# Performance work log

Measured on AMD Instinct MI355X. Metric: run time of the kernel, lower is better.

## Reference

```python
import jax, jax.numpy as jnp
import numpy as np

N = 50000      # nodes
E = 800000     # edges (avg degree 32 w/ 50k nodes -> 16 per direction here)
IN = 128       # in_channels
H = 64         # hidden_channels
G = 64         # graphs in the batch
C = 2          # num_classes


def setup_inputs() -> dict:
    key = jax.random.key(0)
    ks = jax.random.split(key, 8)
    x = jax.random.normal(ks[0], (N, IN), dtype=jnp.float32)
    edge_index = jax.random.randint(ks[1], (2, E), 0, N, dtype=jnp.int64)
    batch = jnp.sort(jax.random.randint(ks[2], (N,), 0, G, dtype=jnp.int64))
    # learned parameters (glorot-ish scale)
    W1 = jax.random.normal(ks[3], (IN, H), dtype=jnp.float32) * (1.0 / np.sqrt(IN))
    b1 = jnp.zeros((H,), dtype=jnp.float32)
    W2 = jax.random.normal(ks[4], (H, H), dtype=jnp.float32) * (1.0 / np.sqrt(H))
    b2 = jnp.zeros((H,), dtype=jnp.float32)
    Wl = jax.random.normal(ks[5], (H, C), dtype=jnp.float32) * (1.0 / np.sqrt(H))
    bl = jnp.zeros((C,), dtype=jnp.float32)
    return {"x": x, "edge_index": edge_index, "batch": batch,
            "W1": W1, "b1": b1, "W2": W2, "b2": b2, "Wl": Wl, "bl": bl}


def _gcn_conv(x, src, dst, W, b, n):
    # PyG GCNConv: linear transform, add self-loops, sym-normalize, scatter-add at dst
    h = x @ W                                   # [n, H]
    loop = jnp.arange(n, dtype=src.dtype)
    s = jnp.concatenate([src, loop])            # [E+n]
    d = jnp.concatenate([dst, loop])
    deg = jax.ops.segment_sum(jnp.ones_like(d, dtype=h.dtype), d, num_segments=n)
    dinv = deg ** -0.5                          # deg >= 1 due to self-loops
    norm = dinv[s] * dinv[d]                    # [E+n]
    msg = h[s] * norm[:, None]                  # gather + scale
    out = jax.ops.segment_sum(msg, d, num_segments=n)  # scatter-add aggregate
    return out + b


def reference(x, edge_index, batch, W1, b1, W2, b2, Wl, bl):
    src, dst = edge_index[0], edge_index[1]
    h = jax.nn.relu(_gcn_conv(x, src, dst, W1, b1, N))
    # dropout is identity in eval mode
    h = jax.nn.relu(_gcn_conv(h, src, dst, W2, b2, N))
    # global mean pool per graph
    counts = jax.ops.segment_sum(jnp.ones((N,), dtype=h.dtype), batch, num_segments=G)
    pooled = jax.ops.segment_sum(h, batch, num_segments=G) / jnp.maximum(counts, 1.0)[:, None]
    out = pooled @ Wl + bl                      # [G, C]
    return (out, pooled)
```

## Files before the change

kernel.cpp:

```cpp
#include <hip/hip_runtime.h>

#define N_NODES   50000
#define N_EDGES   800000
#define IN_CH     128
#define HID       64
#define N_GRAPHS  64
#define N_CLASSES 2
#define NBLK_SCAN ((N_NODES + 255) / 256)
#define NREP      32


#define FILL_CHUNKS ((N_EDGES + 2047) / 2048)
__global__ __launch_bounds__(256) void deg_kernel(const int* __restrict__ ei,
                                                  int* __restrict__ degCount) {
    int part = blockIdx.x & 7;
    int blk  = blockIdx.x >> 3;
    int lo   = part * 6250;
    int hi   = lo + 6250;
#pragma unroll
    for (int it = 0; it < 8; ++it) {
        int e = blk * 2048 + it * 256 + (int)threadIdx.x;
        if (e < N_EDGES) {
            int dst = ei[N_EDGES + e];
            if (dst >= lo && dst < hi) atomicAdd(&degCount[dst], 1);
        }
    }
}

__global__ __launch_bounds__(256) void scan1_kernel(const int* __restrict__ degCount,
                                                    int* __restrict__ blockSums) {
    __shared__ int red[256];
    int i = blockIdx.x * 256 + threadIdx.x;
    red[threadIdx.x] = (i < N_NODES) ? degCount[i] : 0;
    __syncthreads();
    for (int off = 128; off > 0; off >>= 1) {
        if (threadIdx.x < off) red[threadIdx.x] += red[threadIdx.x + off];
        __syncthreads();
    }
    if (threadIdx.x == 0) blockSums[blockIdx.x] = red[0];
}

__global__ __launch_bounds__(256) void scan2_kernel(int* __restrict__ blockSums) {
    __shared__ int s[256];
    int t = threadIdx.x;
    int v = (t < NBLK_SCAN) ? blockSums[t] : 0;
    s[t] = v;
    __syncthreads();
    for (int off = 1; off < 256; off <<= 1) {
        int a = (t >= off) ? s[t - off] : 0;
        __syncthreads();
        s[t] += a;
        __syncthreads();
    }
    if (t < NBLK_SCAN) blockSums[t] = s[t] - v;
}

__global__ __launch_bounds__(256) void scan3_kernel(int* __restrict__ degFill,
                                                    const int* __restrict__ blockSums,
                                                    int* __restrict__ rowPtr,
                                                    float* __restrict__ dinv) {
    __shared__ int s[256];
    int t = threadIdx.x;
    int i = blockIdx.x * 256 + t;
    int d = (i < N_NODES) ? degFill[i] : 0;
    s[t] = d;
    __syncthreads();
    for (int off = 1; off < 256; off <<= 1) {
        int a = (t >= off) ? s[t - off] : 0;
        __syncthreads();
        s[t] += a;
        __syncthreads();
    }
    int excl = s[t] - d + blockSums[blockIdx.x];
    if (i < N_NODES) {
        rowPtr[i]  = excl;
        degFill[i] = excl;
        dinv[i]    = 1.0f / sqrtf((float)(d + 1));
    }
    if (i == 0) rowPtr[N_NODES] = N_EDGES;
}

__global__ __launch_bounds__(256) void fill_kernel(const int* __restrict__ ei,
                                                   int* __restrict__ fillPtr,
                                                   int* __restrict__ colIdx) {
    int part = blockIdx.x & 7;
    int blk  = blockIdx.x >> 3;
    int lo   = part * 6250;
    int hi   = lo + 6250;
#pragma unroll
    for (int it = 0; it < 8; ++it) {
        int e = blk * 2048 + it * 256 + (int)threadIdx.x;
        if (e < N_EDGES) {
            int dst = ei[N_EDGES + e];
            if (dst >= lo && dst < hi) {
                int src = ei[e];
                int pos = atomicAdd(&fillPtr[dst], 1);
                colIdx[pos] = src;
            }
        }
    }
}

#define FMA4(xs, w, a) { (a).x = fmaf((xs), (w).x, (a).x); \
                         (a).y = fmaf((xs), (w).y, (a).y); \
                         (a).z = fmaf((xs), (w).z, (a).z); \
                         (a).w = fmaf((xs), (w).w, (a).w); }

template <int K>
__global__ __launch_bounds__(256) void gemm_kernel(const float* __restrict__ A,
                                                   const float* __restrict__ W,
                                                   const float* __restrict__ dinv,
                                                   float* __restrict__ out) {
    __shared__ float4 Ws[K * 16];
    for (int i = threadIdx.x; i < K * 16; i += 256)
        Ws[i] = ((const float4*)W)[i];
    __syncthreads();

    const int c4   = threadIdx.x & 15;
    const int rg   = threadIdx.x >> 4;
    const int row0 = blockIdx.x * 128 + rg * 8;

    const float4* ap[8];
#pragma unroll
    for (int r = 0; r < 8; ++r) {
        int rowc = min(row0 + r, N_NODES - 1);
        ap[r] = (const float4*)(A + (size_t)rowc * K);
    }

    float4 acc[8] = {};
    for (int kk = 0; kk < K / 4; ++kk) {
        float4 xv[8];
#pragma unroll
        for (int r = 0; r < 8; ++r) xv[r] = ap[r][kk];
        float4 w;
        w = Ws[(4 * kk + 0) * 16 + c4];
#pragma unroll
        for (int r = 0; r < 8; ++r) FMA4(xv[r].x, w, acc[r]);
        w = Ws[(4 * kk + 1) * 16 + c4];
#pragma unroll
        for (int r = 0; r < 8; ++r) FMA4(xv[r].y, w, acc[r]);
        w = Ws[(4 * kk + 2) * 16 + c4];
#pragma unroll
        for (int r = 0; r < 8; ++r) FMA4(xv[r].z, w, acc[r]);
        w = Ws[(4 * kk + 3) * 16 + c4];
#pragma unroll
        for (int r = 0; r < 8; ++r) FMA4(xv[r].w, w, acc[r]);
    }

#pragma unroll
    for (int r = 0; r < 8; ++r) {
        int row = row0 + r;
        if (row < N_NODES) {
            float dv = dinv[row];
            float4 o = acc[r];
            o.x *= dv; o.y *= dv; o.z *= dv; o.w *= dv;
            ((float4*)(out + (size_t)row * HID))[c4] = o;
        }
    }
}

__global__ __launch_bounds__(256) void agg_kernel(const float* __restrict__ g,
                                                  const float* __restrict__ dinv,
                                                  const int* __restrict__ rowPtr,
                                                  const int* __restrict__ colIdx,
                                                  const float* __restrict__ bias,
                                                  float* __restrict__ out) {
    int lane = threadIdx.x & 63;
    int v = blockIdx.x * 4 + (threadIdx.x >> 6);
    if (v >= N_NODES) return;

    float acc = g[(size_t)v * HID + lane];
    int e  = rowPtr[v];
    int e1 = rowPtr[v + 1];
    for (; e + 3 < e1; e += 4) {
        int u0 = colIdx[e], u1 = colIdx[e + 1], u2 = colIdx[e + 2], u3 = colIdx[e + 3];
        float a0 = g[(size_t)u0 * HID + lane];
        float a1 = g[(size_t)u1 * HID + lane];
        float a2 = g[(size_t)u2 * HID + lane];
        float a3 = g[(size_t)u3 * HID + lane];
        acc += (a0 + a1) + (a2 + a3);
    }
    for (; e < e1; ++e) acc += g[(size_t)colIdx[e] * HID + lane];

    float r = dinv[v] * acc + bias[lane];
    out[(size_t)v * HID + lane] = fmaxf(r, 0.f);
}

__global__ __launch_bounds__(256) void agg2pool_kernel(const float* __restrict__ g,
                                                       const float* __restrict__ dinv,
                                                       const int* __restrict__ rowPtr,
                                                       const int* __restrict__ colIdx,
                                                       const float* __restrict__ bias,
                                                       const int* __restrict__ batch,
                                                       float* __restrict__ pooledSum) {
    int lane = threadIdx.x & 63;
    int v = blockIdx.x * 4 + (threadIdx.x >> 6);
    if (v >= N_NODES) return;

    float acc = g[(size_t)v * HID + lane];
    int e  = rowPtr[v];
    int e1 = rowPtr[v + 1];
    for (; e + 3 < e1; e += 4) {
        int u0 = colIdx[e], u1 = colIdx[e + 1], u2 = colIdx[e + 2], u3 = colIdx[e + 3];
        float a0 = g[(size_t)u0 * HID + lane];
        float a1 = g[(size_t)u1 * HID + lane];
        float a2 = g[(size_t)u2 * HID + lane];
        float a3 = g[(size_t)u3 * HID + lane];
        acc += (a0 + a1) + (a2 + a3);
    }
    for (; e < e1; ++e) acc += g[(size_t)colIdx[e] * HID + lane];

    float r = fmaxf(dinv[v] * acc + bias[lane], 0.f);
    int gid = batch[v];
    int rep = blockIdx.x & (NREP - 1);
    atomicAdd(&pooledSum[(size_t)rep * N_GRAPHS * HID + gid * HID + lane], r);
}

__global__ __launch_bounds__(64) void pool2_kernel(const float* __restrict__ pooledSum,
                                                   const int* __restrict__ batch,
                                                   const float* __restrict__ Wl,
                                                   const float* __restrict__ bl,
                                                   float* __restrict__ dout) {
    int g    = blockIdx.x;
    int lane = threadIdx.x;

    int lo0 = 0, hi = N_NODES;
    while (lo0 < hi) { int mid = (lo0 + hi) >> 1; if (batch[mid] < g) lo0 = mid + 1; else hi = mid; }
    int lo1 = lo0; hi = N_NODES;
    while (lo1 < hi) { int mid = (lo1 + hi) >> 1; if (batch[mid] < g + 1) lo1 = mid + 1; else hi = mid; }
    float cnt = (float)(lo1 - lo0);

    float s = 0.f;
#pragma unroll
    for (int rep = 0; rep < NREP; ++rep)
        s += pooledSum[(size_t)rep * N_GRAPHS * HID + g * HID + lane];

    float p = s / fmaxf(cnt, 1.0f);
    dout[N_GRAPHS * N_CLASSES + g * HID + lane] = p;

    float p0 = p * Wl[lane * N_CLASSES + 0];
    float p1 = p * Wl[lane * N_CLASSES + 1];
#pragma unroll
    for (int off = 32; off > 0; off >>= 1) {
        p0 += __shfl_down(p0, off, 64);
        p1 += __shfl_down(p1, off, 64);
    }
    if (lane == 0) {
        dout[g * N_CLASSES + 0] = p0 + bl[0];
        dout[g * N_CLASSES + 1] = p1 + bl[1];
    }
}

extern "C" void kernel_launch(void* const* d_in, const int* in_sizes, int n_in,
                              void* d_out, int out_size, void* d_ws, size_t ws_size,
                              hipStream_t stream) {
    const float* x     = (const float*)d_in[0];
    const int*   ei    = (const int*)d_in[1];
    const int*   batch = (const int*)d_in[2];
    const float* W1    = (const float*)d_in[3];
    const float* b1    = (const float*)d_in[4];
    const float* W2    = (const float*)d_in[5];
    const float* b2    = (const float*)d_in[6];
    const float* Wl    = (const float*)d_in[7];
    const float* bl    = (const float*)d_in[8];
    float* out = (float*)d_out;

    char* ws = (char*)d_ws;
    size_t off = 0;
    auto alloc = [&](size_t bytes) -> void* {
        void* p = ws + off;
        off += (bytes + 255) & ~(size_t)255;
        return p;
    };
    int*   degFill   = (int*)  alloc((size_t)N_NODES * 4);
    int*   rowPtr    = (int*)  alloc((size_t)(N_NODES + 1) * 4);
    float* dinv      = (float*)alloc((size_t)N_NODES * 4);
    int*   blockSums = (int*)  alloc((size_t)NBLK_SCAN * 4);
    float* pooledSum = (float*)alloc((size_t)NREP * N_GRAPHS * HID * 4);
    int*   colIdx    = (int*)  alloc((size_t)N_EDGES * 4);
    float* bufA      = (float*)alloc((size_t)N_NODES * HID * 4);
    float* bufB      = (float*)alloc((size_t)N_NODES * HID * 4);

    hipMemsetAsync(degFill, 0, (size_t)N_NODES * 4, stream);
    hipMemsetAsync(pooledSum, 0, (size_t)NREP * N_GRAPHS * HID * 4, stream);

    deg_kernel  <<<FILL_CHUNKS * 8, 256, 0, stream>>>(ei, degFill);
    scan1_kernel<<<NBLK_SCAN, 256, 0, stream>>>(degFill, blockSums);
    scan2_kernel<<<1, 256, 0, stream>>>(blockSums);
    scan3_kernel<<<NBLK_SCAN, 256, 0, stream>>>(degFill, blockSums, rowPtr, dinv);
    fill_kernel <<<FILL_CHUNKS * 8, 256, 0, stream>>>(ei, degFill, colIdx);

    gemm_kernel<IN_CH><<<(N_NODES + 127) / 128, 256, 0, stream>>>(x, W1, dinv, bufA);
    agg_kernel        <<<N_NODES / 4, 256, 0, stream>>>(bufA, dinv, rowPtr, colIdx, b1, bufB);

    gemm_kernel<HID>  <<<(N_NODES + 127) / 128, 256, 0, stream>>>(bufB, W2, dinv, bufA);
    agg2pool_kernel   <<<N_NODES / 4, 256, 0, stream>>>(bufA, dinv, rowPtr, colIdx, b2, batch, pooledSum);

    pool2_kernel<<<N_GRAPHS, 64, 0, stream>>>(pooledSum, batch, Wl, bl, out);
}
```

Measured before the change: 302.6 us.

## Fuse degree counting with first GEMM and move dinv scaling into aggregation

Merges the degree-count kernel and the first x@W1 GEMM into one launch, with separate block ranges doing each job. This is possible because the GEMM no longer needs dinv; layer-1 aggregation instead multiplies each gathered neighbour row by dinv[u]. Both aggregation loops now unroll by 8, with masked tail handling and two accumulators, to raise memory-level parallelism. The cost is an extra dinv gather per edge in agg1 and wasted loads for padded lanes in the tail.

Result: slower. 320.3 us (+5.9%).

```diff
diff --git a/kernel.cpp b/kernel.cpp
--- a/kernel.cpp
+++ b/kernel.cpp
@@ -8,22 +8,77 @@
 #define N_CLASSES 2
 #define NBLK_SCAN ((N_NODES + 255) / 256)
 #define NREP      32
-
-
 #define FILL_CHUNKS ((N_EDGES + 2047) / 2048)
-__global__ __launch_bounds__(256) void deg_kernel(const int* __restrict__ ei,
-                                                  int* __restrict__ degCount) {
-    int part = blockIdx.x & 7;
-    int blk  = blockIdx.x >> 3;
-    int lo   = part * 6250;
-    int hi   = lo + 6250;
-#pragma unroll
-    for (int it = 0; it < 8; ++it) {
-        int e = blk * 2048 + it * 256 + (int)threadIdx.x;
-        if (e < N_EDGES) {
-            int dst = ei[N_EDGES + e];
-            if (dst >= lo && dst < hi) atomicAdd(&degCount[dst], 1);
-        }
+#define DEG_BLOCKS (FILL_CHUNKS * 8)
+
+
+#define FMA4(xs, w, a) { (a).x = fmaf((xs), (w).x, (a).x); \
+                         (a).y = fmaf((xs), (w).y, (a).y); \
+                         (a).z = fmaf((xs), (w).z, (a).z); \
+                         (a).w = fmaf((xs), (w).w, (a).w); }
+
+__global__ __launch_bounds__(256) void deg_gemm1_kernel(const int* __restrict__ ei,
+                                                        int* __restrict__ degCount,
+                                                        const float* __restrict__ x,
+                                                        const float* __restrict__ W1,
+                                                        float* __restrict__ gg) {
+    __shared__ float4 Ws[IN_CH * 16];
+    if (blockIdx.x < DEG_BLOCKS) {
+        int part = blockIdx.x & 7;
+        int blk  = blockIdx.x >> 3;
+        int lo   = part * 6250;
+        int hi   = lo + 6250;
+#pragma unroll
+        for (int it = 0; it < 8; ++it) {
+            int e = blk * 2048 + it * 256 + (int)threadIdx.x;
+            if (e < N_EDGES) {
+                int dst = ei[N_EDGES + e];
+                if (dst >= lo && dst < hi) atomicAdd(&degCount[dst], 1);
+            }
+        }
+        return;
+    }
+    int bid = blockIdx.x - DEG_BLOCKS;
+    for (int i = threadIdx.x; i < IN_CH * 16; i += 256)
+        Ws[i] = ((const float4*)W1)[i];
+    __syncthreads();
+
+    const int c4   = threadIdx.x & 15;
+    const int rg   = threadIdx.x >> 4;
+    const int row0 = bid * 128 + rg * 8;
+
+    const float4* ap[8];
+#pragma unroll
+    for (int r = 0; r < 8; ++r) {
+        int rowc = min(row0 + r, N_NODES - 1);
+        ap[r] = (const float4*)(x + (size_t)rowc * IN_CH);
+    }
+
+    float4 acc[8] = {};
+    for (int kk = 0; kk < IN_CH / 4; ++kk) {
+        float4 xv[8];
+#pragma unroll
+        for (int r = 0; r < 8; ++r) xv[r] = ap[r][kk];
+        float4 w;
+        w = Ws[(4 * kk + 0) * 16 + c4];
+#pragma unroll
+        for (int r = 0; r < 8; ++r) FMA4(xv[r].x, w, acc[r]);
+        w = Ws[(4 * kk + 1) * 16 + c4];
+#pragma unroll
+        for (int r = 0; r < 8; ++r) FMA4(xv[r].y, w, acc[r]);
+        w = Ws[(4 * kk + 2) * 16 + c4];
+#pragma unroll
+        for (int r = 0; r < 8; ++r) FMA4(xv[r].z, w, acc[r]);
+        w = Ws[(4 * kk + 3) * 16 + c4];
+#pragma unroll
+        for (int r = 0; r < 8; ++r) FMA4(xv[r].w, w, acc[r]);
+    }
+
+#pragma unroll
+    for (int r = 0; r < 8; ++r) {
+        int row = row0 + r;
+        if (row < N_NODES)
+            ((float4*)(gg + (size_t)row * HID))[c4] = acc[r];
     }
 }
 
@@ -101,11 +156,6 @@
     }
 }
 
-#define FMA4(xs, w, a) { (a).x = fmaf((xs), (w).x, (a).x); \
-                         (a).y = fmaf((xs), (w).y, (a).y); \
-                         (a).z = fmaf((xs), (w).z, (a).z); \
-                         (a).w = fmaf((xs), (w).w, (a).w); }
-
 template <int K>
 __global__ __launch_bounds__(256) void gemm_kernel(const float* __restrict__ A,
                                                    const float* __restrict__ W,
@@ -159,30 +209,38 @@
     }
 }
 
-__global__ __launch_bounds__(256) void agg_kernel(const float* __restrict__ g,
-                                                  const float* __restrict__ dinv,
-                                                  const int* __restrict__ rowPtr,
-                                                  const int* __restrict__ colIdx,
-                                                  const float* __restrict__ bias,
-                                                  float* __restrict__ out) {
+__global__ __launch_bounds__(256) void agg1_kernel(const float* __restrict__ gg,
+                                                   const float* __restrict__ dinv,
+                                                   const int* __restrict__ rowPtr,
+                                                   const int* __restrict__ colIdx,
+                                                   const float* __restrict__ bias,
+                                                   float* __restrict__ out) {
     int lane = threadIdx.x & 63;
     int v = blockIdx.x * 4 + (threadIdx.x >> 6);
     if (v >= N_NODES) return;
 
-    float acc = g[(size_t)v * HID + lane];
-    int e  = rowPtr[v];
+    const float dv = dinv[v];
+    float accA = dv * gg[(size_t)v * HID + lane];
+    float accB = 0.f;
+    int e0 = rowPtr[v];
     int e1 = rowPtr[v + 1];
-    for (; e + 3 < e1; e += 4) {
-        int u0 = colIdx[e], u1 = colIdx[e + 1], u2 = colIdx[e + 2], u3 = colIdx[e + 3];
-        float a0 = g[(size_t)u0 * HID + lane];
-        float a1 = g[(size_t)u1 * HID + lane];
-        float a2 = g[(size_t)u2 * HID + lane];
-        float a3 = g[(size_t)u3 * HID + lane];
-        acc += (a0 + a1) + (a2 + a3);
-    }
-    for (; e < e1; ++e) acc += g[(size_t)colIdx[e] * HID + lane];
-
-    float r = dinv[v] * acc + bias[lane];
+    for (int e = e0; e < e1; e += 8) {
+        int   u[8];
+        float du[8];
+#pragma unroll
+        for (int i = 0; i < 8; ++i) {
+            int idx = min(e + i, e1 - 1);
+            u[i]  = colIdx[idx];
+            du[i] = (e + i < e1) ? dinv[u[i]] : 0.f;
+        }
+#pragma unroll
+        for (int i = 0; i < 8; ++i) {
+            float a = gg[(size_t)u[i] * HID + lane];
+            if (i & 1) accB = fmaf(du[i], a, accB);
+            else       accA = fmaf(du[i], a, accA);
+        }
+    }
+    float r = dv * (accA + accB) + bias[lane];
     out[(size_t)v * HID + lane] = fmaxf(r, 0.f);
 }
 
@@ -197,20 +255,27 @@
     int v = blockIdx.x * 4 + (threadIdx.x >> 6);
     if (v >= N_NODES) return;
 
-    float acc = g[(size_t)v * HID + lane];
-    int e  = rowPtr[v];
+    float accA = g[(size_t)v * HID + lane];
+    float accB = 0.f;
+    int e0 = rowPtr[v];
     int e1 = rowPtr[v + 1];
-    for (; e + 3 < e1; e += 4) {
-        int u0 = colIdx[e], u1 = colIdx[e + 1], u2 = colIdx[e + 2], u3 = colIdx[e + 3];
-        float a0 = g[(size_t)u0 * HID + lane];
-        float a1 = g[(size_t)u1 * HID + lane];
-        float a2 = g[(size_t)u2 * HID + lane];
-        float a3 = g[(size_t)u3 * HID + lane];
-        acc += (a0 + a1) + (a2 + a3);
-    }
-    for (; e < e1; ++e) acc += g[(size_t)colIdx[e] * HID + lane];
-
-    float r = fmaxf(dinv[v] * acc + bias[lane], 0.f);
+    for (int e = e0; e < e1; e += 8) {
+        int   u[8];
+        float wsel[8];
+#pragma unroll
+        for (int i = 0; i < 8; ++i) {
+            int idx = min(e + i, e1 - 1);
+            u[i]    = colIdx[idx];
+            wsel[i] = (e + i < e1) ? 1.f : 0.f;
+        }
+#pragma unroll
+        for (int i = 0; i < 8; ++i) {
+            float a = g[(size_t)u[i] * HID + lane];
+            if (i & 1) accB = fmaf(wsel[i], a, accB);
+            else       accA = fmaf(wsel[i], a, accA);
+        }
+    }
+    float r = fmaxf(dinv[v] * (accA + accB) + bias[lane], 0.f);
     int gid = batch[v];
     int rep = blockIdx.x & (NREP - 1);
     atomicAdd(&pooledSum[(size_t)rep * N_GRAPHS * HID + gid * HID + lane], r);
@@ -284,17 +349,17 @@
     hipMemsetAsync(degFill, 0, (size_t)N_NODES * 4, stream);
     hipMemsetAsync(pooledSum, 0, (size_t)NREP * N_GRAPHS * HID * 4, stream);
 
-    deg_kernel  <<<FILL_CHUNKS * 8, 256, 0, stream>>>(ei, degFill);
+    deg_gemm1_kernel<<<DEG_BLOCKS + (N_NODES + 127) / 128, 256, 0, stream>>>(
+        ei, degFill, x, W1, bufA);
     scan1_kernel<<<NBLK_SCAN, 256, 0, stream>>>(degFill, blockSums);
     scan2_kernel<<<1, 256, 0, stream>>>(blockSums);
     scan3_kernel<<<NBLK_SCAN, 256, 0, stream>>>(degFill, blockSums, rowPtr, dinv);
-    fill_kernel <<<FILL_CHUNKS * 8, 256, 0, stream>>>(ei, degFill, colIdx);
-
-    gemm_kernel<IN_CH><<<(N_NODES + 127) / 128, 256, 0, stream>>>(x, W1, dinv, bufA);
-    agg_kernel        <<<N_NODES / 4, 256, 0, stream>>>(bufA, dinv, rowPtr, colIdx, b1, bufB);
-
-    gemm_kernel<HID>  <<<(N_NODES + 127) / 128, 256, 0, stream>>>(bufB, W2, dinv, bufA);
-    agg2pool_kernel   <<<N_NODES / 4, 256, 0, stream>>>(bufA, dinv, rowPtr, colIdx, b2, batch, pooledSum);
+    fill_kernel <<<DEG_BLOCKS, 256, 0, stream>>>(ei, degFill, colIdx);
+
+    agg1_kernel<<<N_NODES / 4, 256, 0, stream>>>(bufA, dinv, rowPtr, colIdx, b1, bufB);
+
+    gemm_kernel<HID><<<(N_NODES + 127) / 128, 256, 0, stream>>>(bufB, W2, dinv, bufA);
+    agg2pool_kernel <<<N_NODES / 4, 256, 0, stream>>>(bufA, dinv, rowPtr, colIdx, b2, batch, pooledSum);
 
     pool2_kernel<<<N_GRAPHS, 64, 0, stream>>>(pooledSum, batch, Wl, bl, out);
 }
```
